# Optimization experiments

Hardware: AMD Instinct MI355X
Metric: run time of the kernel (lower is better)

Reference implementation:

```python
import jax, jax.numpy as jnp
import numpy as np

NCLASS = 8
THRESH = 0.02
POOL_KS = (32, 16, 8)  # ceil(0.5*64), ceil(0.5*32), ceil(0.5*16)
BN_EPS = 1e-5


def _gcn(x, m, W, b):
    A = m + jnp.eye(x.shape[1], dtype=x.dtype)
    dinv = jax.lax.rsqrt(A.sum(-1))
    An = dinv[:, :, None] * A * dinv[:, None, :]
    return jnp.einsum('bij,bjf->bif', An, x @ W) + b


def _sagpool(x, m, w1, w2, b, k):
    # SAGPooling with GraphConv scorer: s = x w1 + (A x) w2 + b; top-k, gate by tanh
    s = (x @ w1 + jnp.einsum('bij,bjf->bif', m, x) @ w2 + b)[..., 0]
    v, idx = jax.lax.top_k(s, k)
    xg = jnp.take_along_axis(x, idx[:, :, None], axis=1) * jnp.tanh(v)[:, :, None]
    mg = jnp.take_along_axis(jnp.take_along_axis(m, idx[:, :, None], 1), idx[:, None, :], 2)
    return xg, mg


def _readout(x):
    return jnp.concatenate([x.max(1), x.mean(1)], axis=-1)  # [gmp || gep]


def _edist(a, b):
    d2 = (a * a).sum(-1)[:, None] + (b * b).sum(-1)[None, :] - 2.0 * (a @ b.T)
    return jnp.sqrt(jnp.clip(d2, 1e-12))


def _conv1d(x, W, b, dil, pad):
    y = jax.lax.conv_general_dilated(x, W, (1,), [(pad, pad)], rhs_dilation=(dil,),
                                     dimension_numbers=('NCH', 'OIH', 'NCH'))
    return jax.nn.relu(y + b[None, :, None])


def _forward(x, labels, idx_train, gat_W, gat_a1, gat_a2, gcn1_W, gcn1_b, gcn2_W, gcn2_b,
             gcn3_W, gcn3_b, pool1_w1, pool1_w2, pool1_b, pool2_w1, pool2_w2, pool2_b,
             pool3_w1, pool3_w2, pool3_b, gru_Wih, gru_Whh, gru_bih, gru_bhh,
             conv1_W, conv1_b, conv2_W, conv2_b, conv3_W, conv3_b,
             fc0_W, fc0_b, bn0_g, bn0_b, fc1_W, fc1_b, att_W1, att_b1, att_W2, att_b2):
    B, C, L = x.shape
    # GAT-style learned adjacency over the C channel-nodes, thresholded to a sparse graph
    h = x @ gat_W
    e = jax.nn.leaky_relu((h @ gat_a1)[:, :, None] + (h @ gat_a2)[:, None, :], 0.2)
    A = jax.nn.softmax(e, axis=-1)
    m = (A > THRESH).astype(x.dtype)  # [B,C,C] block-diagonal-equivalent mask
    # three GCN + SAGPool stages with summed jump-knowledge readout
    g = jax.nn.relu(_gcn(x, m, gcn1_W, gcn1_b))
    g, m = _sagpool(g, m, pool1_w1, pool1_w2, pool1_b, POOL_KS[0])
    r = _readout(g)
    g = jax.nn.relu(_gcn(g, m, gcn2_W, gcn2_b))
    g, m = _sagpool(g, m, pool2_w1, pool2_w2, pool2_b, POOL_KS[1])
    r = r + _readout(g)
    g = jax.nn.relu(_gcn(g, m, gcn3_W, gcn3_b))
    g, m = _sagpool(g, m, pool3_w1, pool3_w2, pool3_b, POOL_KS[2])
    x_gnn = r + _readout(g)  # [B, 2*hidden]
    # GRU: torch nn.GRU(len_ts, gru_dim) with [N,C,L] -> seq axis 0, batch axis 1 (as in source)
    G = gru_Whh.shape[1]
    def step(hprev, xt):
        gi = xt @ gru_Wih.T + gru_bih
        gh = hprev @ gru_Whh.T + gru_bhh
        ir, iz, inn = jnp.split(gi, 3, axis=-1)
        hr, hz, hn = jnp.split(gh, 3, axis=-1)
        rg = jax.nn.sigmoid(ir + hr)
        zg = jax.nn.sigmoid(iz + hz)
        ng = jnp.tanh(inn + rg * hn)
        hnew = (1.0 - zg) * ng + zg * hprev
        return hnew, hnew
    _, ys = jax.lax.scan(step, jnp.zeros((C, G), x.dtype), x)
    x_gru = ys.mean(1)  # [B, G]
    # dilated conv branch; padding = dilation*(kernel-1) both sides as in __init__
    xc = _conv1d(x, conv1_W, conv1_b, 1, 7)
    xc = _conv1d(xc, conv2_W, conv2_b, 2, 8)
    xc = _conv1d(xc, conv3_W, conv3_b, 4, 8)
    x_conv = xc.mean(2)  # [B, filters[2]]
    feat = jnp.concatenate([x_conv, x_gru, x_gnn], axis=1)
    # mapping MLP: Linear -> BatchNorm(train stats) -> LeakyReLU -> Linear
    hm = feat @ fc0_W + fc0_b
    hm = bn0_g * (hm - hm.mean(0)) * jax.lax.rsqrt(hm.var(0) + BN_EPS) + bn0_b
    hm = jax.nn.leaky_relu(hm, 0.01)
    z = hm @ fc1_W + fc1_b  # [B, 128]
    # per-class attention-weighted prototypes over training samples (masked softmax)
    train = jnp.zeros((B,), bool).at[idx_train].set(True)
    cmask = train[None, :] & (labels[None, :] == jnp.arange(NCLASS)[:, None])
    t = jnp.tanh(jnp.einsum('nd,cda->cna', z, att_W1) + att_b1[:, None, :])
    logits = jnp.einsum('cna,ca->cn', t, att_W2) + att_b2[:, None]
    w = jax.nn.softmax(jnp.where(cmask, logits, -1e30), axis=1)
    proto = w @ z  # [NCLASS, 128]
    pd = jnp.exp(-0.5 * _edist(proto, proto))
    proto_dist = pd.sum() / (NCLASS * (NCLASS - 1) / 2)
    dists = jnp.exp(-0.5 * _edist(z, proto))
    return dists, proto_dist


def setup_inputs() -> dict:
    key = jax.random.key(0)
    ks = iter(jax.random.split(key, 64))
    def rn(shape, s=0.05):
        return jax.random.normal(next(ks), shape, jnp.float32) * s
    B, C, L, H, G, NC, AT, F1 = 256, 64, 512, 128, 128, 8, 64, 128
    inp = {}
    inp['x'] = jax.random.normal(next(ks), (B, C, L), jnp.float32)
    inp['labels'] = jnp.arange(B, dtype=jnp.int32) % NC  # guarantees every class in train split
    inp['idx_train'] = jnp.arange(B // 2, dtype=jnp.int32)
    inp['gat_W'] = rn((L, L)); inp['gat_a1'] = rn((L,)); inp['gat_a2'] = rn((L,))
    inp['gcn1_W'] = rn((L, H)); inp['gcn1_b'] = jnp.zeros((H,), jnp.float32)
    inp['gcn2_W'] = rn((H, H)); inp['gcn2_b'] = jnp.zeros((H,), jnp.float32)
    inp['gcn3_W'] = rn((H, H)); inp['gcn3_b'] = jnp.zeros((H,), jnp.float32)
    for i in (1, 2, 3):
        inp['pool%d_w1' % i] = rn((H, 1)); inp['pool%d_w2' % i] = rn((H, 1))
        inp['pool%d_b' % i] = jnp.zeros((1,), jnp.float32)
    inp['gru_Wih'] = rn((3 * G, L)); inp['gru_Whh'] = rn((3 * G, G))
    inp['gru_bih'] = jnp.zeros((3 * G,), jnp.float32); inp['gru_bhh'] = jnp.zeros((3 * G,), jnp.float32)
    inp['conv1_W'] = rn((F1, C, 8)); inp['conv1_b'] = jnp.zeros((F1,), jnp.float32)
    inp['conv2_W'] = rn((F1, F1, 5)); inp['conv2_b'] = jnp.zeros((F1,), jnp.float32)
    inp['conv3_W'] = rn((F1, F1, 3)); inp['conv3_b'] = jnp.zeros((F1,), jnp.float32)
    inp['fc0_W'] = rn((F1 + G + 2 * H, 256)); inp['fc0_b'] = jnp.zeros((256,), jnp.float32)
    inp['bn0_g'] = jnp.ones((256,), jnp.float32); inp['bn0_b'] = jnp.zeros((256,), jnp.float32)
    inp['fc1_W'] = rn((256, 128)); inp['fc1_b'] = jnp.zeros((128,), jnp.float32)
    inp['att_W1'] = rn((NC, 128, AT)); inp['att_b1'] = jnp.zeros((NC, AT), jnp.float32)
    inp['att_W2'] = rn((NC, AT)); inp['att_b2'] = jnp.zeros((NC,), jnp.float32)
    return inp


def reference(x, labels, idx_train, gat_W, gat_a1, gat_a2, gcn1_W, gcn1_b, gcn2_W, gcn2_b,
              gcn3_W, gcn3_b, pool1_w1, pool1_w2, pool1_b, pool2_w1, pool2_w2, pool2_b,
              pool3_w1, pool3_w2, pool3_b, gru_Wih, gru_Whh, gru_bih, gru_bhh,
              conv1_W, conv1_b, conv2_W, conv2_b, conv3_W, conv3_b,
              fc0_W, fc0_b, bn0_g, bn0_b, fc1_W, fc1_b, att_W1, att_b1, att_W2, att_b2):
    return _forward(x, labels, idx_train, gat_W, gat_a1, gat_a2, gcn1_W, gcn1_b, gcn2_W, gcn2_b,
                    gcn3_W, gcn3_b, pool1_w1, pool1_w2, pool1_b, pool2_w1, pool2_w2, pool2_b,
                    pool3_w1, pool3_w2, pool3_b, gru_Wih, gru_Whh, gru_bih, gru_bhh,
                    conv1_W, conv1_b, conv2_W, conv2_b, conv3_W, conv3_b,
                    fc0_W, fc0_b, bn0_g, bn0_b, fc1_W, fc1_b, att_W1, att_b1, att_W2, att_b2)
```

## Files before the change

kernel.cpp:

```cpp
#include <hip/hip_runtime.h>
#include <math.h>

#define BB 256
#define CC 64
#define LL 512
#define HH 128
#define G3 384
#define NC 8
#define AT 64
#define CL1 519
#define CL2 527
#define CL3 535
#define THRESH 0.02f

typedef _Float16 h2 __attribute__((ext_vector_type(2)));
typedef _Float16 f16x8 __attribute__((ext_vector_type(8)));
typedef float f32x4 __attribute__((ext_vector_type(4)));
union HU { unsigned int u; h2 h; float f; };
union BU { uint4 u; f16x8 h; };

__device__ inline float warp_red_sum(float v) {
  #pragma unroll
  for (int o = 32; o > 0; o >>= 1) v += __shfl_down(v, o, 64);
  return v;
}
__device__ inline float warp_allred_max(float v) {
  #pragma unroll
  for (int o = 32; o > 0; o >>= 1) v = fmaxf(v, __shfl_xor(v, o, 64));
  return v;
}
__device__ inline float warp_allred_sum(float v) {
  #pragma unroll
  for (int o = 32; o > 0; o >>= 1) v += __shfl_xor(v, o, 64);
  return v;
}

__device__ inline float fdot2f(h2 a, h2 b, float c) {
#if __has_builtin(__builtin_amdgcn_fdot2)
  return __builtin_amdgcn_fdot2(a, b, c, false);
#else
  float r;
  asm volatile("v_dot2_f32_f16 %0, %1, %2, %3" : "=v"(r) : "v"(a), "v"(b), "v"(c));
  return r;
#endif
}
__device__ inline h2 asH2(float f) { HU u; u.f = f; return u.h; }
__device__ inline h2 uH2(unsigned int x) { HU u; u.u = x; return u.h; }
__device__ inline unsigned int packh(float a, float b) {
  HU u; h2 t; t.x = (_Float16)a; t.y = (_Float16)b; u.h = t; return u.u;
}
__device__ inline float vexp2(float x) { float r; asm("v_exp_f32 %0, %1" : "=v"(r) : "v"(x)); return r; }
__device__ inline float vrcp(float x)  { float r; asm("v_rcp_f32 %0, %1" : "=v"(r) : "v"(x)); return r; }
__device__ inline float fsigm(float x) { return vrcp(1.f + vexp2(-1.44269504f * x)); }
__device__ inline float ftanh(float x) { return 1.f - 2.f * vrcp(vexp2(2.88539008f * x) + 1.f); }

__global__ void k_wa(const float* __restrict__ gatW, const float* __restrict__ a1,
                     const float* __restrict__ a2, float* wa1, float* wa2) {
  int l = blockIdx.x * 64 + threadIdx.x;
  const float* row = gatW + l * LL;
  float s1 = 0.f, s2 = 0.f;
  for (int k = 0; k < LL; k++) { float w = row[k]; s1 += w * a1[k]; s2 += w * a2[k]; }
  wa1[l] = s1; wa2[l] = s2;
}

__global__ void k_ha(const float* __restrict__ x, const float* __restrict__ wa1,
                     const float* __restrict__ wa2, float* ha1, float* ha2) {
  int wid = threadIdx.x >> 6, lane = threadIdx.x & 63;
  int row = blockIdx.x * 4 + wid;
  const float* xr = x + (size_t)row * LL;
  float s1 = 0.f, s2 = 0.f;
  for (int q = lane; q < LL; q += 64) { float v = xr[q]; s1 += v * wa1[q]; s2 += v * wa2[q]; }
  s1 = warp_red_sum(s1); s2 = warp_red_sum(s2);
  if (lane == 0) { ha1[row] = s1; ha2[row] = s2; }
}

__global__ void k_softmask(const float* __restrict__ ha1, const float* __restrict__ ha2,
                           float* __restrict__ mask, float* __restrict__ dinv) {
  int wid = threadIdx.x >> 6, lane = threadIdx.x & 63;
  int row = blockIdx.x * 4 + wid;
  int b = row >> 6;
  float e = ha1[row] + ha2[b * 64 + lane];
  e = e < 0.f ? 0.2f * e : e;
  float mx = warp_allred_max(e);
  float ex = expf(e - mx);
  float sm = warp_allred_sum(ex);
  float A = ex / sm;
  float mval = (A > THRESH) ? 1.0f : 0.0f;
  mask[(size_t)row * 64 + lane] = mval;
  float cnt = warp_allred_sum(mval);
  if (lane == 0) dinv[row] = 1.0f / sqrtf(cnt + 1.0f);
}

__global__ void k_packall(const float* __restrict__ gcnW0, const float* __restrict__ gcnW1,
                          const float* __restrict__ gcnW2, const float* __restrict__ wih,
                          const float* __restrict__ whh,
                          unsigned int* gw1h, unsigned int* gw2h, unsigned int* gw3h,
                          unsigned int* wihTh, unsigned int* wpk) {
  int idx = blockIdx.x * 256 + threadIdx.x;
  if (idx < 32768) {
    int w_ = idx & 3, l = (idx >> 2) & 63, n = (idx >> 8) & 7, c = idx >> 11;
    int k0 = c * 32 + ((l >> 4) << 3) + 2 * w_;
    int col = n * 16 + (l & 15);
    gw1h[idx] = packh(gcnW0[k0 * 128 + col], gcnW0[(k0 + 1) * 128 + col]);
  } else if (idx < 40960) {
    int t = idx - 32768;
    int w_ = t & 3, l = (t >> 2) & 63, n = (t >> 8) & 7, c = t >> 11;
    int k0 = c * 32 + ((l >> 4) << 3) + 2 * w_;
    int col = n * 16 + (l & 15);
    gw2h[t] = packh(gcnW1[k0 * 128 + col], gcnW1[(k0 + 1) * 128 + col]);
  } else if (idx < 49152) {
    int t = idx - 40960;
    int w_ = t & 3, l = (t >> 2) & 63, n = (t >> 8) & 7, c = t >> 11;
    int k0 = c * 32 + ((l >> 4) << 3) + 2 * w_;
    int col = n * 16 + (l & 15);
    gw3h[t] = packh(gcnW2[k0 * 128 + col], gcnW2[(k0 + 1) * 128 + col]);
  } else if (idx < 147456) {
    int t = idx - 49152;
    int w_ = t & 3, l = (t >> 2) & 63;
    int nfc = t >> 8;
    int n = nfc % 24, c = nfc / 24;
    int k0 = c * 32 + ((l >> 4) << 3) + 2 * w_;
    int col = n * 16 + (l & 15);
    wihTh[t] = packh(wih[col * 512 + k0], wih[col * 512 + k0 + 1]);
  } else if (idx < 172032) {
    int t = idx - 147456; int j = t & 127, rk = t >> 7;
    int r = rk >> 6, k2 = rk & 63;
    const float* src = whh + (size_t)(j + 128 * r) * 128 + 2 * k2;
    wpk[t] = packh(src[0], src[1]);
  }
}

__device__ inline void packw_one(const float* __restrict__ W, unsigned int* __restrict__ out,
                                 int idx, int cinlog, int KS) {
  int w_ = idx & 3, l = (idx >> 2) & 63, n = (idx >> 8) & 7, c = idx >> 11;
  int CIN = 1 << cinlog;
  int oc = n * 16 + (l & 15);
  int k0 = c * 32 + ((l >> 4) << 3) + 2 * w_;
  int t0 = k0 >> cinlog, ci0 = k0 & (CIN - 1);
  int t1 = (k0 + 1) >> cinlog, ci1 = (k0 + 1) & (CIN - 1);
  out[idx] = packh(W[(size_t)oc * CIN * KS + ci0 * KS + t0],
                   W[(size_t)oc * CIN * KS + ci1 * KS + t1]);
}
__global__ void k_packw_mfma(const float* __restrict__ c1W, const float* __restrict__ c2W,
                             const float* __restrict__ c3W, unsigned int* o1,
                             unsigned int* o2, unsigned int* o3) {
  int idx = blockIdx.x * 256 + threadIdx.x;
  if (idx < 32768) packw_one(c1W, o1, idx, 6, 8);
  else if (idx < 73728) packw_one(c2W, o2, idx - 32768, 7, 5);
  else if (idx < 98304) packw_one(c3W, o3, idx - 73728, 7, 3);
}

__global__ __launch_bounds__(256) void k_gmfma(const float* __restrict__ A,
                                               const uint4* __restrict__ Bf,
                                               float* __restrict__ C,
                                               int M, int N, int K) {
  __shared__ _Float16 as[2][64 * 64];
  int nwg = gridDim.x, bid = blockIdx.x;
  int lb = (bid & 7) * (nwg >> 3) + (bid >> 3);
  int nbn = N >> 7;
  int bm = lb / nbn, bn = lb - bm * nbn;
  int m0 = bm * 64;
  int tid = threadIdx.x, l = tid & 63, w = tid >> 6;
  int NKT = K >> 6, NC2 = K >> 5, N16 = N >> 4;
  int nf0 = bn * 8 + 2 * w, nf1 = nf0 + 1;
  int ar = tid >> 2;
  int ac = (tid & 3) * 16;
  float4 rg[4];
  auto stageA = [&](int kt) {
    const float* src = &A[(size_t)(m0 + ar) * K + kt * 64 + ac];
    rg[0] = *(const float4*)&src[0];
    rg[1] = *(const float4*)&src[4];
    rg[2] = *(const float4*)&src[8];
    rg[3] = *(const float4*)&src[12];
  };
  auto commitA = [&](int buf) {
    int s0 = (tid & 3) * 2;
    int phys0 = (s0 ^ (ar & 7)) * 8;
    int phys1 = ((s0 + 1) ^ (ar & 7)) * 8;
    uint4 v0, v1;
    v0.x = packh(rg[0].x, rg[0].y); v0.y = packh(rg[0].z, rg[0].w);
    v0.z = packh(rg[1].x, rg[1].y); v0.w = packh(rg[1].z, rg[1].w);
    v1.x = packh(rg[2].x, rg[2].y); v1.y = packh(rg[2].z, rg[2].w);
    v1.z = packh(rg[3].x, rg[3].y); v1.w = packh(rg[3].z, rg[3].w);
    *(uint4*)&as[buf][ar * 64 + phys0] = v0;
    *(uint4*)&as[buf][ar * 64 + phys1] = v1;
  };
  f32x4 acc[4][2];
  #pragma unroll
  for (int m = 0; m < 4; m++) {
    acc[m][0] = (f32x4){0.f, 0.f, 0.f, 0.f};
    acc[m][1] = (f32x4){0.f, 0.f, 0.f, 0.f};
  }
  stageA(0); commitA(0);
  uint4 bc0 = Bf[(size_t)nf0 * 64 + l];
  uint4 bc1 = Bf[(size_t)nf1 * 64 + l];
  __syncthreads();
  for (int c = 0; c < NC2; c++) {
    int kt = c >> 1, half = c & 1;
    if (half == 0 && kt + 1 < NKT) stageA(kt + 1);
    uint4 pn0 = bc0, pn1 = bc1;
    if (c + 1 < NC2) {
      pn0 = Bf[(size_t)((c + 1) * N16 + nf0) * 64 + l];
      pn1 = Bf[(size_t)((c + 1) * N16 + nf1) * 64 + l];
    }
    int slotbase = half * 4 + (l >> 4);
    f16x8 a[4];
    #pragma unroll
    for (int m = 0; m < 4; m++) {
      int row = m * 16 + (l & 15);
      int phys = slotbase ^ (row & 7);
      a[m] = *(const f16x8*)&as[kt & 1][row * 64 + phys * 8];
    }
    BU u0, u1; u0.u = bc0; u1.u = bc1;
    #pragma unroll
    for (int m = 0; m < 4; m++) {
      acc[m][0] = __builtin_amdgcn_mfma_f32_16x16x32_f16(a[m], u0.h, acc[m][0], 0, 0, 0);
      acc[m][1] = __builtin_amdgcn_mfma_f32_16x16x32_f16(a[m], u1.h, acc[m][1], 0, 0, 0);
    }
    if (half == 1 && kt + 1 < NKT) {
      commitA((kt + 1) & 1);
      __syncthreads();
    }
    bc0 = pn0; bc1 = pn1;
  }
  #pragma unroll
  for (int n = 0; n < 2; n++) {
    int col = (nf0 + n) * 16 + (l & 15);
    #pragma unroll
    for (int m = 0; m < 4; m++) {
      #pragma unroll
      for (int i = 0; i < 4; i++) {
        C[(size_t)(m0 + m * 16 + (l >> 4) * 4 + i) * N + col] = acc[m][n][i];
      }
    }
  }
}

__global__ void k_gcnagg(const float* __restrict__ xw, const float* __restrict__ mask,
                         const float* __restrict__ dinv, const float* __restrict__ bias,
                         float* __restrict__ gout, int N) {
  __shared__ float mrow[64], dv[64];
  int b = blockIdx.x / N, i = blockIdx.x % N;
  if (threadIdx.x < N) {
    mrow[threadIdx.x] = mask[(size_t)(b * N + i) * N + threadIdx.x];
    dv[threadIdx.x] = dinv[b * N + threadIdx.x];
  }
  __syncthreads();
  int f = threadIdx.x;
  float di = dv[i];
  float acc = di * xw[(size_t)(b * N + i) * HH + f];
  for (int j = 0; j < N; j++) acc += mrow[j] * dv[j] * xw[(size_t)(b * N + j) * HH + f];
  float y = di * acc + bias[f];
  gout[(size_t)(b * N + i) * HH + f] = y > 0.f ? y : 0.f;
}

__global__ __launch_bounds__(256) void k_pool(const float* __restrict__ g,
                                              const float* __restrict__ mask,
                                              const float* __restrict__ w1,
                                              const float* __restrict__ w2,
                                              const float* __restrict__ pb, int N, int kk,
                                              float* gp, float* mnext, float* dnext,
                                              float* __restrict__ r) {
  __shared__ float gs[64 * 129];
  __shared__ float ms[64 * 65];
  __shared__ float d1s[64], d2s[64], sv[64], vals[32], tvs[32];
  __shared__ int idxs[32];
  int b = blockIdx.x, tid = threadIdx.x;
  for (int q = tid; q < N * 128; q += 256) {
    int row = q >> 7, d = q & 127;
    gs[row * 129 + d] = g[(size_t)(b * N + row) * 128 + d];
  }
  for (int q = tid; q < N * N; q += 256) {
    int row = q / N, u = q - row * N;
    ms[row * 65 + u] = mask[(size_t)(b * N + row) * N + u];
  }
  __syncthreads();
  if (tid < N) {
    float a = 0.f, c = 0.f;
    const float* gr = &gs[tid * 129];
    for (int d = 0; d < 128; d++) { float v = gr[d]; a += v * w1[d]; c += v * w2[d]; }
    d1s[tid] = a; d2s[tid] = c;
  }
  __syncthreads();
  if (tid < N) {
    const float* mr = &ms[tid * 65];
    float s = d1s[tid] + pb[0];
    for (int j = 0; j < N; j++) s += mr[j] * d2s[j];
    sv[tid] = s;
  }
  __syncthreads();
  if (tid < 64) {
    float myv = (tid < N) ? sv[tid] : -3.4e38f;
    int alive = (tid < N) ? 1 : 0;
    for (int t = 0; t < kk; t++) {
      float cv = alive ? myv : -3.4e38f;
      int ci = tid;
      #pragma unroll
      for (int o = 32; o > 0; o >>= 1) {
        float ov = __shfl_xor(cv, o, 64);
        int oi = __shfl_xor(ci, o, 64);
        if (ov > cv || (ov == cv && oi < ci)) { cv = ov; ci = oi; }
      }
      if (tid == ci) alive = 0;
      if (tid == 0) { idxs[t] = ci; vals[t] = cv; }
    }
  }
  __syncthreads();
  if (tid < kk) tvs[tid] = tanhf(vals[tid]);
  __syncthreads();
  if (tid < HH) {
    float mx = -3.4e38f, sm = 0.f;
    for (int t = 0; t < kk; t++) {
      float v = gs[idxs[t] * 129 + tid] * tvs[t];
      if (gp) gp[(size_t)(b * kk + t) * HH + tid] = v;
      mx = fmaxf(mx, v); sm += v;
    }
    r[b * 256 + tid] += mx;
    r[b * 256 + 128 + tid] += sm / (float)kk;
  }
  for (int q = tid; q < kk * kk; q += 256) {
    int t = q / kk, u = q - t * kk;
    mnext[(size_t)(b * kk + t) * kk + u] = ms[idxs[t] * 65 + idxs[u]];
  }
  if (dnext && tid < kk) {
    float s = 0.f;
    for (int u = 0; u < kk; u++) s += ms[idxs[tid] * 65 + idxs[u]];
    dnext[b * kk + tid] = 1.0f / sqrtf(s + 1.0f);
  }
}

__global__ __launch_bounds__(256, 1) void k_gru(const float* __restrict__ gi,
                                                const unsigned int* __restrict__ wpk,
                                                const float* __restrict__ bhh,
                                                const float* __restrict__ bih,
                                                float* __restrict__ ys) {
  __shared__ _Float16 hb[2][128];
  int c = blockIdx.x;
  int j = threadIdx.x >> 1, half = threadIdx.x & 1;
  int kb = half * 32;
  h2 w0[32], w1[32], w2[32];
  #pragma unroll
  for (int kk = 0; kk < 32; kk++) { HU u; u.u = wpk[(kb + kk) * 128 + j]; w0[kk] = u.h; }
  #pragma unroll
  for (int kk = 0; kk < 32; kk++) { HU u; u.u = wpk[(64 + kb + kk) * 128 + j]; w1[kk] = u.h; }
  #pragma unroll
  for (int kk = 0; kk < 32; kk++) { HU u; u.u = wpk[(128 + kb + kk) * 128 + j]; w2[kk] = u.h; }
  float bh0 = bhh[j], bh1 = bhh[j + 128], bh2 = bhh[j + 256];
  float bi0 = bih[j], bi1 = bih[j + 128], bi2 = bih[j + 256];
  float hprev = 0.f;
  if (half == 0) hb[0][j] = (_Float16)0.f;
  __syncthreads();
  const float* gbase = gi + (size_t)c * G3 + j;
  float g0 = gbase[0], g1 = gbase[128], g2 = gbase[256];
  int cur = 0;
  for (int b = 0; b < BB; b++) {
    float n0 = 0.f, n1 = 0.f, n2 = 0.f;
    if (b + 1 < BB) {
      const float* gn = gbase + (size_t)(b + 1) * CC * G3;
      n0 = gn[0]; n1 = gn[128]; n2 = gn[256];
    }
    float a0a = 0.f, a0b = 0.f, a1a = 0.f, a1b = 0.f, a2a = 0.f, a2b = 0.f;
    #pragma unroll
    for (int q = 0; q < 8; q++) {
      float4 hv = *(const float4*)&hb[cur][half * 64 + q * 8];
      h2 h0 = asH2(hv.x), h1 = asH2(hv.y), h2v = asH2(hv.z), h3 = asH2(hv.w);
      a0a = fdot2f(w0[q * 4 + 0], h0, a0a); a0b = fdot2f(w0[q * 4 + 1], h1, a0b);
      a0a = fdot2f(w0[q * 4 + 2], h2v, a0a); a0b = fdot2f(w0[q * 4 + 3], h3, a0b);
      a1a = fdot2f(w1[q * 4 + 0], h0, a1a); a1b = fdot2f(w1[q * 4 + 1], h1, a1b);
      a1a = fdot2f(w1[q * 4 + 2], h2v, a1a); a1b = fdot2f(w1[q * 4 + 3], h3, a1b);
      a2a = fdot2f(w2[q * 4 + 0], h0, a2a); a2b = fdot2f(w2[q * 4 + 1], h1, a2b);
      a2a = fdot2f(w2[q * 4 + 2], h2v, a2a); a2b = fdot2f(w2[q * 4 + 3], h3, a2b);
    }
    float A0 = a0a + a0b, A1 = a1a + a1b, A2 = a2a + a2b;
    A0 += __shfl_xor(A0, 1, 64);
    A1 += __shfl_xor(A1, 1, 64);
    A2 += __shfl_xor(A2, 1, 64);
    A0 += bh0; A1 += bh1; A2 += bh2;
    float rg = fsigm(g0 + bi0 + A0);
    float zg = fsigm(g1 + bi1 + A1);
    float ng = ftanh(g2 + bi2 + rg * A2);
    float hn = (1.f - zg) * ng + zg * hprev;
    hprev = hn;
    if (half == 0) {
      ys[(size_t)(b * CC + c) * 128 + j] = hn;
      hb[cur ^ 1][j] = (_Float16)hn;
    }
    asm volatile("s_waitcnt lgkmcnt(0)" ::: "memory");
    __builtin_amdgcn_s_barrier();
    cur ^= 1;
    g0 = n0; g1 = n1; g2 = n2;
  }
}

__global__ void k_grumean(const float* __restrict__ ys, float* __restrict__ xgru) {
  int b = blockIdx.x, u = threadIdx.x;
  float acc = 0.f;
  for (int c = 0; c < CC; c++) acc += ys[(size_t)(b * CC + c) * 128 + u];
  xgru[b * 128 + u] = acc / 64.f;
}

template<int CIN, int KS, int DIL, int PAD, int LIN, int LOUT, int MODE>
__global__ __launch_bounds__(256) void k_cmfma(const void* __restrict__ inv,
                                               const uint4* __restrict__ Bf,
                                               const float* __restrict__ bias,
                                               void* __restrict__ outv, int b0) {
  constexpr int QN = CIN / 32;
  constexpr int NCH = KS * QN;
  constexpr int SLOTS = CIN / 8;
  constexpr int NT = (LOUT + 63) / 64;
  __shared__ _Float16 xs[72 * CIN];
  int nb = blockIdx.x / NT;
  int p0 = (blockIdx.x % NT) * 64;
  int tid = threadIdx.x;
  int l = tid & 63, w = tid >> 6;

  if constexpr (MODE == 0) {
    const float* src = (const float*)inv + (size_t)nb * CIN * LIN;
    for (int q = tid; q < (CIN / 2) * 72; q += 256) {
      int ci2 = q / 72, r = q % 72;
      int ci = 2 * ci2;
      int p = p0 - PAD + r;
      float v0 = 0.f, v1 = 0.f;
      if (p >= 0 && p < LIN) { v0 = src[ci * LIN + p]; v1 = src[(ci + 1) * LIN + p]; }
      int slot = ci >> 3;
      int phys = slot ^ (r & 7);
      *(unsigned int*)&xs[r * CIN + phys * 8 + (ci & 7)] = packh(v0, v1);
    }
  } else {
    const _Float16* src = (const _Float16*)inv + (size_t)nb * LIN * CIN;
    for (int q = tid; q < 72 * SLOTS; q += 256) {
      int r = q / SLOTS, s = q % SLOTS;
      int p = p0 - PAD + r;
      uint4 v = make_uint4(0u, 0u, 0u, 0u);
      if (p >= 0 && p < LIN) v = *(const uint4*)&src[(size_t)p * CIN + s * 8];
      int phys = s ^ (r & 7);
      *(uint4*)&xs[r * CIN + phys * 8] = v;
    }
  }
  __syncthreads();

  int n0 = 2 * w, n1 = n0 + 1;
  f32x4 acc[4][2];
  #pragma unroll
  for (int m = 0; m < 4; m++) {
    acc[m][0] = (f32x4){0.f, 0.f, 0.f, 0.f};
    acc[m][1] = (f32x4){0.f, 0.f, 0.f, 0.f};
  }
  uint4 bc0 = Bf[(size_t)(0 * 8 + n0) * 64 + l];
  uint4 bc1 = Bf[(size_t)(0 * 8 + n1) * 64 + l];
  for (int c = 0; c < NCH; c++) {
    uint4 bn0 = bc0, bn1 = bc1;
    if (c + 1 < NCH) {
      bn0 = Bf[(size_t)((c + 1) * 8 + n0) * 64 + l];
      bn1 = Bf[(size_t)((c + 1) * 8 + n1) * 64 + l];
    }
    int t = c / QN, q = c % QN;
    int slotbase = q * 4 + (l >> 4);
    f16x8 a[4];
    #pragma unroll
    for (int m = 0; m < 4; m++) {
      int r = m * 16 + (l & 15) + t * DIL;
      int phys = slotbase ^ (r & 7);
      a[m] = *(const f16x8*)&xs[r * CIN + phys * 8];
    }
    BU u0, u1; u0.u = bc0; u1.u = bc1;
    #pragma unroll
    for (int m = 0; m < 4; m++) {
      acc[m][0] = __builtin_amdgcn_mfma_f32_16x16x32_f16(a[m], u0.h, acc[m][0], 0, 0, 0);
      acc[m][1] = __builtin_amdgcn_mfma_f32_16x16x32_f16(a[m], u1.h, acc[m][1], 0, 0, 0);
    }
    bc0 = bn0; bc1 = bn1;
  }

  if constexpr (MODE == 2) {
    float* xcv = (float*)outv;
    #pragma unroll
    for (int n = 0; n < 2; n++) {
      int oc = (2 * w + n) * 16 + (l & 15);
      float bz = bias[oc];
      float s = 0.f;
      #pragma unroll
      for (int m = 0; m < 4; m++) {
        #pragma unroll
        for (int i = 0; i < 4; i++) {
          int pos = p0 + m * 16 + (l >> 4) * 4 + i;
          if (pos < LOUT) { float y = acc[m][n][i] + bz; s += y > 0.f ? y : 0.f; }
        }
      }
      s += __shfl_xor(s, 16, 64);
      s += __shfl_xor(s, 32, 64);
      if (l < 16) atomicAdd(&xcv[(size_t)(b0 + nb) * 128 + oc], s);
    }
  } else {
    _Float16* outp = (_Float16*)outv + (size_t)nb * LOUT * 128;
    #pragma unroll
    for (int n = 0; n < 2; n++) {
      int oc = (2 * w + n) * 16 + (l & 15);
      float bz = bias[oc];
      #pragma unroll
      for (int m = 0; m < 4; m++) {
        #pragma unroll
        for (int i = 0; i < 4; i++) {
          int pos = p0 + m * 16 + (l >> 4) * 4 + i;
          if (pos < LOUT) {
            float y = acc[m][n][i] + bz;
            outp[(size_t)pos * 128 + oc] = (_Float16)(y > 0.f ? y : 0.f);
          }
        }
      }
    }
  }
}

__global__ void k_fc0(const float* __restrict__ xconv, const float* __restrict__ xgru,
                      const float* __restrict__ r, const float* __restrict__ W,
                      const float* __restrict__ bias, float* __restrict__ hm) {
  __shared__ float feat[512];
  int b = blockIdx.x, t = threadIdx.x;
  if (t < 128) { feat[t] = xconv[b * 128 + t] * (1.f / (float)CL3); feat[128 + t] = xgru[b * 128 + t]; }
  feat[256 + t] = r[b * 256 + t];
  __syncthreads();
  float acc = bias[t];
  for (int k = 0; k < 512; k++) acc += feat[k] * W[k * 256 + t];
  hm[b * 256 + t] = acc;
}

__global__ void k_bn(const float* __restrict__ hm, const float* __restrict__ gamma,
                     const float* __restrict__ beta, float* __restrict__ out) {
  __shared__ float red[256];
  int n = blockIdx.x, t = threadIdx.x;
  float v = hm[t * 256 + n];
  red[t] = v; __syncthreads();
  for (int s = 128; s > 0; s >>= 1) { if (t < s) red[t] += red[t + s]; __syncthreads(); }
  float mean = red[0] / 256.f; __syncthreads();
  float dv = v - mean;
  red[t] = dv * dv; __syncthreads();
  for (int s = 128; s > 0; s >>= 1) { if (t < s) red[t] += red[t + s]; __syncthreads(); }
  float var = red[0] / 256.f;
  float y = gamma[n] * dv * (1.f / sqrtf(var + 1e-5f)) + beta[n];
  out[t * 256 + n] = y < 0.f ? 0.01f * y : y;
}

__global__ void k_fc1(const float* __restrict__ hmn, const float* __restrict__ W,
                      const float* __restrict__ bias, float* __restrict__ z) {
  __shared__ float hs[256];
  int b = blockIdx.x, t = threadIdx.x;
  hs[t] = hmn[b * 256 + t]; hs[128 + t] = hmn[b * 256 + 128 + t];
  __syncthreads();
  float acc = bias[t];
  for (int k = 0; k < 256; k++) acc += hs[k] * W[k * 128 + t];
  z[b * 128 + t] = acc;
}

__global__ __launch_bounds__(256) void k_att1(const float* __restrict__ z,
                                              const float* __restrict__ W1,
                                              const float* __restrict__ b1,
                                              const float* __restrict__ W2,
                                              float* __restrict__ logits) {
  __shared__ float sa[32][64];
  __shared__ float sb[32][64];
  int c = blockIdx.x >> 2;
  int m0 = (blockIdx.x & 3) * 64;
  const float* B = W1 + (size_t)c * 128 * AT;
  int tx = threadIdx.x & 15, ty = threadIdx.x >> 4;
  float acc[4][4];
  #pragma unroll
  for (int i = 0; i < 4; i++)
    #pragma unroll
    for (int j = 0; j < 4; j++) acc[i][j] = 0.f;
  int arow = threadIdx.x >> 2;
  int acol = (threadIdx.x & 3) * 8;
  int brow = threadIdx.x >> 4;
  int bcol = (threadIdx.x & 15) * 4;
  for (int k0 = 0; k0 < 128; k0 += 32) {
    float4 av0 = *(const float4*)&z[(size_t)(m0 + arow) * 128 + k0 + acol];
    float4 av1 = *(const float4*)&z[(size_t)(m0 + arow) * 128 + k0 + acol + 4];
    float4 bv0 = *(const float4*)&B[(size_t)(k0 + brow) * AT + bcol];
    float4 bv1 = *(const float4*)&B[(size_t)(k0 + brow + 16) * AT + bcol];
    __syncthreads();
    sa[acol + 0][arow] = av0.x; sa[acol + 1][arow] = av0.y;
    sa[acol + 2][arow] = av0.z; sa[acol + 3][arow] = av0.w;
    sa[acol + 4][arow] = av1.x; sa[acol + 5][arow] = av1.y;
    sa[acol + 6][arow] = av1.z; sa[acol + 7][arow] = av1.w;
    *(float4*)&sb[brow][bcol] = bv0;
    *(float4*)&sb[brow + 16][bcol] = bv1;
    __syncthreads();
    #pragma unroll
    for (int kk = 0; kk < 32; kk++) {
      float4 a4 = *(const float4*)&sa[kk][ty * 4];
      float4 b4 = *(const float4*)&sb[kk][tx * 4];
      acc[0][0] += a4.x * b4.x; acc[0][1] += a4.x * b4.y; acc[0][2] += a4.x * b4.z; acc[0][3] += a4.x * b4.w;
      acc[1][0] += a4.y * b4.x; acc[1][1] += a4.y * b4.y; acc[1][2] += a4.y * b4.z; acc[1][3] += a4.y * b4.w;
      acc[2][0] += a4.z * b4.x; acc[2][1] += a4.z * b4.y; acc[2][2] += a4.z * b4.z; acc[2][3] += a4.z * b4.w;
      acc[3][0] += a4.w * b4.x; acc[3][1] += a4.w * b4.y; acc[3][2] += a4.w * b4.z; acc[3][3] += a4.w * b4.w;
    }
  }
  const float* b1c = b1 + c * AT;
  const float* w2c = W2 + c * AT;
  float w2v[4], b1v[4];
  #pragma unroll
  for (int j = 0; j < 4; j++) { w2v[j] = w2c[tx * 4 + j]; b1v[j] = b1c[tx * 4 + j]; }
  #pragma unroll
  for (int i = 0; i < 4; i++) {
    float s = 0.f;
    #pragma unroll
    for (int j = 0; j < 4; j++) s += tanhf(acc[i][j] + b1v[j]) * w2v[j];
    #pragma unroll
    for (int o = 8; o > 0; o >>= 1) s += __shfl_xor(s, o, 64);
    if (tx == 0) logits[c * 256 + m0 + ty * 4 + i] = s;
  }
}

__global__ void k_att2(const float* __restrict__ z, const int* __restrict__ labels,
                       const int* __restrict__ idx_train, int ntrain,
                       const float* __restrict__ logits, const float* __restrict__ b2,
                       float* __restrict__ protos) {
  __shared__ float wv[256], red[256];
  __shared__ int trainm[256];
  int c = blockIdx.x, n = threadIdx.x;
  trainm[n] = 0; __syncthreads();
  if (n < ntrain) trainm[idx_train[n]] = 1;
  __syncthreads();
  bool keep = trainm[n] && (labels[n] == c);
  float ml = keep ? (logits[c * 256 + n] + b2[c]) : -1e30f;
  red[n] = ml; __syncthreads();
  for (int s = 128; s > 0; s >>= 1) { if (n < s) red[n] = fmaxf(red[n], red[n + s]); __syncthreads(); }
  float mx = red[0]; __syncthreads();
  float e = expf(ml - mx);
  wv[n] = e; red[n] = e; __syncthreads();
  for (int s = 128; s > 0; s >>= 1) { if (n < s) red[n] += red[n + s]; __syncthreads(); }
  float ssum = red[0]; __syncthreads();
  wv[n] = wv[n] / ssum;
  __syncthreads();
  if (n < 128) {
    float p = 0.f;
    for (int q = 0; q < 256; q++) p += wv[q] * z[q * 128 + n];
    protos[c * 128 + n] = p;
  }
}

__global__ void k_dist(const float* __restrict__ z, const float* __restrict__ protos,
                       float* __restrict__ dout) {
  if (blockIdx.x == BB) {
    int t = threadIdx.x;
    if (t < 64) {
      int i = t >> 3, jx = t & 7;
      float dot = 0.f, p2i = 0.f, p2j = 0.f;
      for (int d = 0; d < 128; d++) {
        float a = protos[i * 128 + d], bb2 = protos[jx * 128 + d];
        dot += a * bb2; p2i += a * a; p2j += bb2 * bb2;
      }
      float d2 = fmaxf(p2i + p2j - 2.f * dot, 1e-12f);
      float e = expf(-0.5f * sqrtf(d2));
      e = warp_red_sum(e);
      if (t == 0) dout[2048] = e / 28.f;
    }
    return;
  }
  __shared__ float zs[128], red[128];
  int n = blockIdx.x, t = threadIdx.x;
  zs[t] = z[n * 128 + t];
  red[t] = zs[t] * zs[t]; __syncthreads();
  for (int s = 64; s > 0; s >>= 1) { if (t < s) red[t] += red[t + s]; __syncthreads(); }
  float z2 = red[0];
  if (t < NC) {
    float dot = 0.f, p2 = 0.f;
    const float* pr = protos + t * 128;
    for (int d = 0; d < 128; d++) { float pv = pr[d]; dot += pv * zs[d]; p2 += pv * pv; }
    float d2 = fmaxf(z2 + p2 - 2.f * dot, 1e-12f);
    dout[n * NC + t] = expf(-0.5f * sqrtf(d2));
  }
}

extern "C" void kernel_launch(void* const* d_in, const int* in_sizes, int n_in,
                              void* d_out, int out_size, void* d_ws, size_t ws_size,
                              hipStream_t stream) {
  const float* x = (const float*)d_in[0];
  const int* labels = (const int*)d_in[1];
  const int* idx_train = (const int*)d_in[2];
  const float* gat_W = (const float*)d_in[3];
  const float* gat_a1 = (const float*)d_in[4];
  const float* gat_a2 = (const float*)d_in[5];
  const float* gcnW[3] = {(const float*)d_in[6], (const float*)d_in[8], (const float*)d_in[10]};
  const float* gcnB[3] = {(const float*)d_in[7], (const float*)d_in[9], (const float*)d_in[11]};
  const float* pw1[3] = {(const float*)d_in[12], (const float*)d_in[15], (const float*)d_in[18]};
  const float* pw2[3] = {(const float*)d_in[13], (const float*)d_in[16], (const float*)d_in[19]};
  const float* pbb[3] = {(const float*)d_in[14], (const float*)d_in[17], (const float*)d_in[20]};
  const float* wih = (const float*)d_in[21];
  const float* whh = (const float*)d_in[22];
  const float* bih = (const float*)d_in[23];
  const float* bhh = (const float*)d_in[24];
  const float* c1W = (const float*)d_in[25]; const float* c1b = (const float*)d_in[26];
  const float* c2W = (const float*)d_in[27]; const float* c2b = (const float*)d_in[28];
  const float* c3W = (const float*)d_in[29]; const float* c3b = (const float*)d_in[30];
  const float* fc0W = (const float*)d_in[31]; const float* fc0b = (const float*)d_in[32];
  const float* bn0g = (const float*)d_in[33]; const float* bn0b = (const float*)d_in[34];
  const float* fc1W = (const float*)d_in[35]; const float* fc1b = (const float*)d_in[36];
  const float* aW1 = (const float*)d_in[37]; const float* ab1 = (const float*)d_in[38];
  const float* aW2 = (const float*)d_in[39]; const float* ab2 = (const float*)d_in[40];
  float* out = (float*)d_out;
  float* ws = (float*)d_ws;

  size_t off = 0;
  auto take = [&](size_t n) { size_t o = off; off += (n + 63) & ~(size_t)63; return o; };
  float* wa1   = ws + take(512);
  float* wa2   = ws + take(512);
  float* ha1   = ws + take(BB * CC);
  float* ha2   = ws + take(BB * CC);
  float* dinv  = ws + take(BB * 64);
  float* rbuf  = ws + take(BB * 256);
  float* xgru  = ws + take(BB * 128);
  float* xconv = ws + take(BB * 128);
  float* hm    = ws + take(BB * 256);
  float* hmn   = ws + take(BB * 256);
  float* zb    = ws + take(BB * 128);
  float* protos = ws + take(NC * 128);
  float* lgts  = ws + take(NC * 256);
  float* gw1h  = ws + take(256 * 128);
  float* gw2h  = ws + take(64 * 128);
  float* gw3h  = ws + take(64 * 128);
  float* wpkf  = ws + take(192 * 128);
  float* wslot = ws + take(512 * 384);
  float* Z     = ws + take(8568832);
  float* mA  = Z;
  float* mB  = Z + 1048576;
  float* xw  = Z + 2097152;
  float* gb  = Z + 4194304;
  float* gp1 = Z + 6291456;
  float* gp2 = Z + 7340032;
  float* gi = Z;
  float* ys = Z + 6291456;
  float* cv1 = Z;
  float* cv2 = Z + 4251648;
  unsigned int* wpk = (unsigned int*)wpkf;
  unsigned int* wihTh = (unsigned int*)wslot;
  unsigned int* wt1h = (unsigned int*)wslot;
  unsigned int* wt2h = wt1h + 32768;
  unsigned int* wt3h = wt2h + 40960;

  hipMemsetAsync(rbuf, 0, BB * 256 * sizeof(float), stream);
  hipMemsetAsync(xconv, 0, BB * 128 * sizeof(float), stream);

  k_wa<<<8, 64, 0, stream>>>(gat_W, gat_a1, gat_a2, wa1, wa2);
  k_packall<<<672, 256, 0, stream>>>(gcnW[0], gcnW[1], gcnW[2], wih, whh,
                                     (unsigned int*)gw1h, (unsigned int*)gw2h,
                                     (unsigned int*)gw3h, wihTh, wpk);
  k_ha<<<BB * CC / 4, 256, 0, stream>>>(x, wa1, wa2, ha1, ha2);
  k_softmask<<<BB * 64 / 4, 256, 0, stream>>>(ha1, ha2, mA, dinv);

  const int Ns[3] = {64, 32, 16};
  const int ks[3] = {32, 16, 8};
  const int Kin[3] = {512, 128, 128};
  const float* gins[3] = {x, gp1, gp2};
  const unsigned int* gwh[3] = {(unsigned int*)gw1h, (unsigned int*)gw2h, (unsigned int*)gw3h};
  float* mcur[3] = {mA, mB, mA};
  float* mnxt[3] = {mB, mA, mB};
  float* gps[3]  = {gp1, gp2, nullptr};
  for (int s = 0; s < 3; s++) {
    int N = Ns[s];
    k_gmfma<<<(BB * N / 64), 256, 0, stream>>>(
        gins[s], (const uint4*)gwh[s], xw, BB * N, HH, Kin[s]);
    k_gcnagg<<<BB * N, 128, 0, stream>>>(xw, mcur[s], dinv, gcnB[s], gb, N);
    k_pool<<<BB, 256, 0, stream>>>(gb, mcur[s], pw1[s], pw2[s], pbb[s], N, ks[s],
                                   gps[s], mnxt[s], s < 2 ? dinv : nullptr, rbuf);
  }

  k_gmfma<<<(BB * CC / 64) * 3, 256, 0, stream>>>(
      x, (const uint4*)wihTh, gi, BB * CC, G3, LL);
  k_gru<<<CC, 256, 0, stream>>>(gi, wpk, bhh, bih, ys);
  k_grumean<<<BB, 128, 0, stream>>>(ys, xgru);

  k_packw_mfma<<<384, 256, 0, stream>>>(c1W, c2W, c3W, wt1h, wt2h, wt3h);
  for (int bc = 0; bc < 2; bc++) {
    int b0 = bc * 128;
    k_cmfma<64, 8, 1, 7, 512, CL1, 0><<<128 * 9, 256, 0, stream>>>(
        x + (size_t)b0 * CC * LL, (const uint4*)wt1h, c1b, cv1, b0);
    k_cmfma<128, 5, 2, 8, CL1, CL2, 1><<<128 * 9, 256, 0, stream>>>(
        cv1, (const uint4*)wt2h, c2b, cv2, b0);
    k_cmfma<128, 3, 4, 8, CL2, CL3, 2><<<128 * 9, 256, 0, stream>>>(
        cv2, (const uint4*)wt3h, c3b, xconv, b0);
  }

  k_fc0<<<BB, 256, 0, stream>>>(xconv, xgru, rbuf, fc0W, fc0b, hm);
  k_bn<<<256, 256, 0, stream>>>(hm, bn0g, bn0b, hmn);
  k_fc1<<<BB, 128, 0, stream>>>(hmn, fc1W, fc1b, zb);
  k_att1<<<NC * 4, 256, 0, stream>>>(zb, aW1, ab1, aW2, lgts);
  k_att2<<<NC, 256, 0, stream>>>(zb, labels, idx_train, in_sizes[2], lgts, ab2, protos);
  k_dist<<<BB + 1, 128, 0, stream>>>(zb, protos, out);
}
```

Baseline: 486.2 us.

## Overlap GRU recurrence with conv stages by co-launching them in mega kernels

The 256-step sequential GRU, which ran alone on only 64 blocks, is split into 12 chunks. Each chunk runs inside a fused kernel whose first 64 blocks advance the recurrence while the remaining blocks compute a conv1d stage, with hidden state carried across launches through a global buffer. The GRU input projection and hidden outputs are also stored in fp16, which halves that traffic, and the per-batch GRU mean is folded into fc0 so one kernel disappears. The risks are lower precision in the gate inputs and outputs, and the conv work is now split into 4 batch chunks instead of 2, which means more launches.

New measurement: 576.4 us. 1.19x slower.

```diff
diff --git a/kernel.cpp b/kernel.cpp
--- a/kernel.cpp
+++ b/kernel.cpp
@@ -152,8 +152,8 @@
 
 __global__ __launch_bounds__(256) void k_gmfma(const float* __restrict__ A,
                                                const uint4* __restrict__ Bf,
-                                               float* __restrict__ C,
-                                               int M, int N, int K) {
+                                               void* __restrict__ Cv,
+                                               int M, int N, int K, int out16) {
   __shared__ _Float16 as[2][64 * 64];
   int nwg = gridDim.x, bid = blockIdx.x;
   int lb = (bid & 7) * (nwg >> 3) + (bid >> 3);
@@ -223,14 +223,28 @@
     }
     bc0 = pn0; bc1 = pn1;
   }
-  #pragma unroll
-  for (int n = 0; n < 2; n++) {
-    int col = (nf0 + n) * 16 + (l & 15);
-    #pragma unroll
-    for (int m = 0; m < 4; m++) {
+  if (out16) {
+    _Float16* Ch = (_Float16*)Cv;
+    #pragma unroll
+    for (int n = 0; n < 2; n++) {
+      int col = (nf0 + n) * 16 + (l & 15);
       #pragma unroll
-      for (int i = 0; i < 4; i++) {
-        C[(size_t)(m0 + m * 16 + (l >> 4) * 4 + i) * N + col] = acc[m][n][i];
+      for (int m = 0; m < 4; m++) {
+        #pragma unroll
+        for (int i = 0; i < 4; i++)
+          Ch[(size_t)(m0 + m * 16 + (l >> 4) * 4 + i) * N + col] = (_Float16)acc[m][n][i];
+      }
+    }
+  } else {
+    float* Cf = (float*)Cv;
+    #pragma unroll
+    for (int n = 0; n < 2; n++) {
+      int col = (nf0 + n) * 16 + (l & 15);
+      #pragma unroll
+      for (int m = 0; m < 4; m++) {
+        #pragma unroll
+        for (int i = 0; i < 4; i++)
+          Cf[(size_t)(m0 + m * 16 + (l >> 4) * 4 + i) * N + col] = acc[m][n][i];
       }
     }
   }
@@ -329,14 +343,13 @@
   }
 }
 
-__global__ __launch_bounds__(256, 1) void k_gru(const float* __restrict__ gi,
-                                                const unsigned int* __restrict__ wpk,
-                                                const float* __restrict__ bhh,
-                                                const float* __restrict__ bih,
-                                                float* __restrict__ ys) {
-  __shared__ _Float16 hb[2][128];
-  int c = blockIdx.x;
-  int j = threadIdx.x >> 1, half = threadIdx.x & 1;
+__device__ void gru_slice(int c, const _Float16* __restrict__ gi,
+                          const unsigned int* __restrict__ wpk,
+                          const float* __restrict__ bhh, const float* __restrict__ bih,
+                          _Float16* __restrict__ ys, float* __restrict__ hglob,
+                          int step0, int nsteps, _Float16* hb) {
+  int tid = threadIdx.x;
+  int j = tid >> 1, half = tid & 1;
   int kb = half * 32;
   h2 w0[32], w1[32], w2[32];
   #pragma unroll
@@ -347,22 +360,26 @@
   for (int kk = 0; kk < 32; kk++) { HU u; u.u = wpk[(128 + kb + kk) * 128 + j]; w2[kk] = u.h; }
   float bh0 = bhh[j], bh1 = bhh[j + 128], bh2 = bhh[j + 256];
   float bi0 = bih[j], bi1 = bih[j + 128], bi2 = bih[j + 256];
-  float hprev = 0.f;
-  if (half == 0) hb[0][j] = (_Float16)0.f;
-  __syncthreads();
-  const float* gbase = gi + (size_t)c * G3 + j;
-  float g0 = gbase[0], g1 = gbase[128], g2 = gbase[256];
+  float hprev = (step0 == 0) ? 0.f : hglob[c * 128 + j];
+  if (half == 0) hb[j] = (_Float16)hprev;
+  __syncthreads();
+  const _Float16* gbase = gi + (size_t)c * G3 + j;
+  size_t stride = (size_t)CC * G3;
+  float g0 = (float)gbase[(size_t)step0 * stride];
+  float g1 = (float)gbase[(size_t)step0 * stride + 128];
+  float g2 = (float)gbase[(size_t)step0 * stride + 256];
   int cur = 0;
-  for (int b = 0; b < BB; b++) {
+  for (int s = 0; s < nsteps; s++) {
+    int b = step0 + s;
     float n0 = 0.f, n1 = 0.f, n2 = 0.f;
-    if (b + 1 < BB) {
-      const float* gn = gbase + (size_t)(b + 1) * CC * G3;
-      n0 = gn[0]; n1 = gn[128]; n2 = gn[256];
+    if (s + 1 < nsteps) {
+      const _Float16* gn = gbase + (size_t)(b + 1) * stride;
+      n0 = (float)gn[0]; n1 = (float)gn[128]; n2 = (float)gn[256];
     }
     float a0a = 0.f, a0b = 0.f, a1a = 0.f, a1b = 0.f, a2a = 0.f, a2b = 0.f;
     #pragma unroll
     for (int q = 0; q < 8; q++) {
-      float4 hv = *(const float4*)&hb[cur][half * 64 + q * 8];
+      float4 hv = *(const float4*)&hb[cur * 128 + half * 64 + q * 8];
       h2 h0 = asH2(hv.x), h1 = asH2(hv.y), h2v = asH2(hv.z), h3 = asH2(hv.w);
       a0a = fdot2f(w0[q * 4 + 0], h0, a0a); a0b = fdot2f(w0[q * 4 + 1], h1, a0b);
       a0a = fdot2f(w0[q * 4 + 2], h2v, a0a); a0b = fdot2f(w0[q * 4 + 3], h3, a0b);
@@ -382,35 +399,27 @@
     float hn = (1.f - zg) * ng + zg * hprev;
     hprev = hn;
     if (half == 0) {
-      ys[(size_t)(b * CC + c) * 128 + j] = hn;
-      hb[cur ^ 1][j] = (_Float16)hn;
+      ys[(size_t)(b * CC + c) * 128 + j] = (_Float16)hn;
+      hb[(cur ^ 1) * 128 + j] = (_Float16)hn;
     }
     asm volatile("s_waitcnt lgkmcnt(0)" ::: "memory");
     __builtin_amdgcn_s_barrier();
     cur ^= 1;
     g0 = n0; g1 = n1; g2 = n2;
   }
-}
-
-__global__ void k_grumean(const float* __restrict__ ys, float* __restrict__ xgru) {
-  int b = blockIdx.x, u = threadIdx.x;
-  float acc = 0.f;
-  for (int c = 0; c < CC; c++) acc += ys[(size_t)(b * CC + c) * 128 + u];
-  xgru[b * 128 + u] = acc / 64.f;
+  if (half == 0) hglob[c * 128 + j] = hprev;
 }
 
 template<int CIN, int KS, int DIL, int PAD, int LIN, int LOUT, int MODE>
-__global__ __launch_bounds__(256) void k_cmfma(const void* __restrict__ inv,
-                                               const uint4* __restrict__ Bf,
-                                               const float* __restrict__ bias,
-                                               void* __restrict__ outv, int b0) {
+__device__ void conv_body(int bid, const void* __restrict__ inv,
+                          const uint4* __restrict__ Bf, const float* __restrict__ bias,
+                          void* __restrict__ outv, int b0, _Float16* xs) {
   constexpr int QN = CIN / 32;
   constexpr int NCH = KS * QN;
   constexpr int SLOTS = CIN / 8;
   constexpr int NT = (LOUT + 63) / 64;
-  __shared__ _Float16 xs[72 * CIN];
-  int nb = blockIdx.x / NT;
-  int p0 = (blockIdx.x % NT) * 64;
+  int nb = bid / NT;
+  int p0 = (bid % NT) * 64;
   int tid = threadIdx.x;
   int l = tid & 63, w = tid >> 6;
 
@@ -512,12 +521,39 @@
   }
 }
 
-__global__ void k_fc0(const float* __restrict__ xconv, const float* __restrict__ xgru,
+template<int CIN, int KS, int DIL, int PAD, int LIN, int LOUT, int MODE>
+__global__ __launch_bounds__(256) void k_mega(const _Float16* __restrict__ gi,
+                                              const unsigned int* __restrict__ wpk,
+                                              const float* __restrict__ bhh,
+                                              const float* __restrict__ bih,
+                                              _Float16* __restrict__ ys,
+                                              float* __restrict__ hglob,
+                                              int step0, int nsteps,
+                                              const void* __restrict__ inv,
+                                              const uint4* __restrict__ Bf,
+                                              const float* __restrict__ bias,
+                                              void* __restrict__ outv, int b0) {
+  constexpr int XSN = (72 * CIN) > 256 ? (72 * CIN) : 256;
+  __shared__ _Float16 smem[XSN];
+  if ((int)blockIdx.x < CC) {
+    gru_slice(blockIdx.x, gi, wpk, bhh, bih, ys, hglob, step0, nsteps, smem);
+  } else {
+    conv_body<CIN, KS, DIL, PAD, LIN, LOUT, MODE>(blockIdx.x - CC, inv, Bf, bias, outv, b0, smem);
+  }
+}
+
+__global__ void k_fc0(const float* __restrict__ xconv, const _Float16* __restrict__ ys,
                       const float* __restrict__ r, const float* __restrict__ W,
                       const float* __restrict__ bias, float* __restrict__ hm) {
   __shared__ float feat[512];
   int b = blockIdx.x, t = threadIdx.x;
-  if (t < 128) { feat[t] = xconv[b * 128 + t] * (1.f / (float)CL3); feat[128 + t] = xgru[b * 128 + t]; }
+  if (t < 128) {
+    feat[t] = xconv[b * 128 + t] * (1.f / (float)CL3);
+    const _Float16* yb = ys + (size_t)b * CC * 128 + t;
+    float acc = 0.f;
+    for (int c = 0; c < CC; c++) acc += (float)yb[c * 128];
+    feat[128 + t] = acc / 64.f;
+  }
   feat[256 + t] = r[b * 256 + t];
   __syncthreads();
   float acc = bias[t];
@@ -709,13 +745,13 @@
   float* ha2   = ws + take(BB * CC);
   float* dinv  = ws + take(BB * 64);
   float* rbuf  = ws + take(BB * 256);
-  float* xgru  = ws + take(BB * 128);
   float* xconv = ws + take(BB * 128);
   float* hm    = ws + take(BB * 256);
   float* hmn   = ws + take(BB * 256);
   float* zb    = ws + take(BB * 128);
   float* protos = ws + take(NC * 128);
   float* lgts  = ws + take(NC * 256);
+  float* hglob = ws + take(CC * 128);
   float* gw1h  = ws + take(256 * 128);
   float* gw2h  = ws + take(64 * 128);
   float* gw3h  = ws + take(64 * 128);
@@ -728,10 +764,10 @@
   float* gb  = Z + 4194304;
   float* gp1 = Z + 6291456;
   float* gp2 = Z + 7340032;
-  float* gi = Z;
-  float* ys = Z + 6291456;
-  float* cv1 = Z;
-  float* cv2 = Z + 4251648;
+  _Float16* gih = (_Float16*)Z;
+  _Float16* ysh = (_Float16*)(Z + 3145728);
+  float* cv1 = Z + 4194304;
+  float* cv2 = Z + 6320128;
   unsigned int* wpk = (unsigned int*)wpkf;
   unsigned int* wihTh = (unsigned int*)wslot;
   unsigned int* wt1h = (unsigned int*)wslot;
@@ -759,29 +795,35 @@
   for (int s = 0; s < 3; s++) {
     int N = Ns[s];
     k_gmfma<<<(BB * N / 64), 256, 0, stream>>>(
-        gins[s], (const uint4*)gwh[s], xw, BB * N, HH, Kin[s]);
+        gins[s], (const uint4*)gwh[s], xw, BB * N, HH, Kin[s], 0);
     k_gcnagg<<<BB * N, 128, 0, stream>>>(xw, mcur[s], dinv, gcnB[s], gb, N);
     k_pool<<<BB, 256, 0, stream>>>(gb, mcur[s], pw1[s], pw2[s], pbb[s], N, ks[s],
                                    gps[s], mnxt[s], s < 2 ? dinv : nullptr, rbuf);
   }
 
   k_gmfma<<<(BB * CC / 64) * 3, 256, 0, stream>>>(
-      x, (const uint4*)wihTh, gi, BB * CC, G3, LL);
-  k_gru<<<CC, 256, 0, stream>>>(gi, wpk, bhh, bih, ys);
-  k_grumean<<<BB, 128, 0, stream>>>(ys, xgru);
-
+      x, (const uint4*)wihTh, gih, BB * CC, G3, LL, 1);
   k_packw_mfma<<<384, 256, 0, stream>>>(c1W, c2W, c3W, wt1h, wt2h, wt3h);
-  for (int bc = 0; bc < 2; bc++) {
-    int b0 = bc * 128;
-    k_cmfma<64, 8, 1, 7, 512, CL1, 0><<<128 * 9, 256, 0, stream>>>(
+
+  const int nst[12] = {22, 22, 22, 22, 21, 21, 21, 21, 21, 21, 21, 21};
+  int s0 = 0, mi = 0;
+  for (int ck = 0; ck < 4; ck++) {
+    int b0 = ck * 64;
+    k_mega<64, 8, 1, 7, 512, CL1, 0><<<CC + 64 * 9, 256, 0, stream>>>(
+        gih, wpk, bhh, bih, ysh, hglob, s0, nst[mi],
         x + (size_t)b0 * CC * LL, (const uint4*)wt1h, c1b, cv1, b0);
-    k_cmfma<128, 5, 2, 8, CL1, CL2, 1><<<128 * 9, 256, 0, stream>>>(
+    s0 += nst[mi++];
+    k_mega<128, 5, 2, 8, CL1, CL2, 1><<<CC + 64 * 9, 256, 0, stream>>>(
+        gih, wpk, bhh, bih, ysh, hglob, s0, nst[mi],
         cv1, (const uint4*)wt2h, c2b, cv2, b0);
-    k_cmfma<128, 3, 4, 8, CL2, CL3, 2><<<128 * 9, 256, 0, stream>>>(
+    s0 += nst[mi++];
+    k_mega<128, 3, 4, 8, CL2, CL3, 2><<<CC + 64 * 9, 256, 0, stream>>>(
+        gih, wpk, bhh, bih, ysh, hglob, s0, nst[mi],
         cv2, (const uint4*)wt3h, c3b, xconv, b0);
-  }
-
-  k_fc0<<<BB, 256, 0, stream>>>(xconv, xgru, rbuf, fc0W, fc0b, hm);
+    s0 += nst[mi++];
+  }
+
+  k_fc0<<<BB, 256, 0, stream>>>(xconv, ysh, rbuf, fc0W, fc0b, hm);
   k_bn<<<256, 256, 0, stream>>>(hm, bn0g, bn0b, hmn);
   k_fc1<<<BB, 128, 0, stream>>>(hmn, fc1W, fc1b, zb);
   k_att1<<<NC * 4, 256, 0, stream>>>(zb, aW1, ab1, aW2, lgts);
```
